# Optimization experiments

Hardware: AMD Instinct MI355X
Metric: run time of the kernel (lower is better)

The kernel has to match this reference:

```python
import jax, jax.numpy as jnp
import numpy as np

N_NODES = 50000
N_EDGES = 800000
NODE_DIM = 128
EDGE_DIM = 16
OUT_DIM = 64
HEADS = 4


def setup_inputs() -> dict:
    key = jax.random.key(0)
    ks = jax.random.split(key, 12)
    x = jax.random.normal(ks[0], (N_NODES, NODE_DIM), jnp.float32)
    edge_index = jax.random.randint(ks[1], (2, N_EDGES), 0, N_NODES)
    batch = jnp.zeros((N_NODES,), jnp.int32)
    edge_attr = jax.random.normal(ks[2], (N_EDGES, EDGE_DIM), jnp.float32)
    s = 1.0 / np.sqrt(NODE_DIM)
    W = jax.random.normal(ks[3], (NODE_DIM, HEADS * OUT_DIM), jnp.float32) * s
    att_src = jax.random.normal(ks[4], (HEADS, OUT_DIM), jnp.float32) * 0.1
    att_dst = jax.random.normal(ks[5], (HEADS, OUT_DIM), jnp.float32) * 0.1
    W_e = jax.random.normal(ks[6], (EDGE_DIM, HEADS * OUT_DIM), jnp.float32) * (1.0 / np.sqrt(EDGE_DIM))
    att_edge = jax.random.normal(ks[7], (HEADS, OUT_DIM), jnp.float32) * 0.1
    bias = jnp.zeros((OUT_DIM,), jnp.float32)
    gamma = jnp.ones((OUT_DIM,), jnp.float32)
    beta = jnp.zeros((OUT_DIM,), jnp.float32)
    return {"x": x, "edge_index": edge_index, "batch": batch, "edge_attr": edge_attr,
            "W": W, "att_src": att_src, "att_dst": att_dst, "W_e": W_e,
            "att_edge": att_edge, "bias": bias, "gamma": gamma, "beta": beta}


def reference(x, edge_index, batch, edge_attr, W, att_src, att_dst, W_e, att_edge, bias, gamma, beta):
    N = x.shape[0]
    H, C = att_src.shape
    src, dst = edge_index[0], edge_index[1]
    E = src.shape[0]

    # add self loops; self-loop edge_attr = per-node mean of incoming edge attrs (PyG fill_value='mean')
    cnt = jax.ops.segment_sum(jnp.ones((E, 1), x.dtype), dst, num_segments=N)
    loop_attr = jax.ops.segment_sum(edge_attr, dst, num_segments=N) / jnp.maximum(cnt, 1.0)
    loop_idx = jnp.arange(N, dtype=src.dtype)
    src_f = jnp.concatenate([src, loop_idx])
    dst_f = jnp.concatenate([dst, loop_idx])
    ea = jnp.concatenate([edge_attr, loop_attr], axis=0)

    h = (x @ W).reshape(N, H, C)                       # [N,H,C]
    a_src = jnp.einsum('nhc,hc->nh', h, att_src)       # [N,H]
    a_dst = jnp.einsum('nhc,hc->nh', h, att_dst)
    e_emb = (ea @ W_e).reshape(-1, H, C)               # [E',H,C]
    a_edge = jnp.einsum('ehc,hc->eh', e_emb, att_edge)

    alpha = jax.nn.leaky_relu(a_src[src_f] + a_dst[dst_f] + a_edge, 0.2)  # [E',H]
    amax = jax.ops.segment_max(alpha, dst_f, num_segments=N)
    expa = jnp.exp(alpha - amax[dst_f])
    denom = jax.ops.segment_sum(expa, dst_f, num_segments=N)
    att = expa / (denom[dst_f] + 1e-16)                # segment softmax over dst

    msg = h[src_f] * att[:, :, None]                   # [E',H,C]
    out = jax.ops.segment_sum(msg, dst_f, num_segments=N)  # [N,H,C]
    out = out.mean(axis=1) + bias                      # concat=False -> head mean

    mu = out.mean(-1, keepdims=True)
    var = out.var(-1, keepdims=True)
    out = (out - mu) / jnp.sqrt(var + 1e-5) * gamma + beta
    return jax.nn.elu(out)
```

## Files before the change

### kernel.cpp

```cpp
#include <hip/hip_runtime.h>

typedef unsigned int u32;
typedef unsigned short u16;

static constexpr int NN  = 50000;
static constexpr int EE  = 800000;
static constexpr int CAP = 64;

typedef __attribute__((ext_vector_type(8))) short bf16x8;
typedef __attribute__((ext_vector_type(4))) float f32x4;

__device__ inline float u2f(u32 u){ union{u32 i; float f;} v; v.i=u; return v.f; }
__device__ inline float bf2f(u16 u){ return u2f(((u32)u)<<16); }
__device__ inline u16 f2bf(float f){ union{float f; u32 i;} v; v.f=f; u32 i=v.i;
    return (u16)((i + 0x7fffu + ((i>>16)&1u))>>16); }
__device__ inline u32 pk2(float a, float b){ return (u32)f2bf(a) | ((u32)f2bf(b)<<16); }
__device__ inline float lrelu(float x){ return x > 0.f ? x : 0.2f*x; }

__device__ inline float ld(const void* base, size_t i, int f32m){
    return f32m ? ((const float*)base)[i] : bf2f(((const u16*)base)[i]);
}

__device__ inline float wsum(float v){
    #pragma unroll
    for (int m=1;m<64;m<<=1) v += __shfl_xor(v, m, 64);
    return v;
}

#if defined(__has_builtin)
#if __has_builtin(__builtin_amdgcn_fdot2_f32_bf16)
#define HAS_DOT2 1
#endif
#endif

#ifdef HAS_DOT2
typedef __attribute__((ext_vector_type(2))) __bf16 bf16x2;
#endif

__device__ inline float dot2acc(u32 hv, u32 wv, float acc){
#ifdef HAS_DOT2
    union { u32 u; bf16x2 v; } a, b; a.u = hv; b.u = wv;
    return __builtin_amdgcn_fdot2_f32_bf16(a.v, b.v, acc, false);
#else
    acc = fmaf(u2f(hv<<16),         u2f(wv<<16),         acc);
    acc = fmaf(u2f(hv&0xffff0000u), u2f(wv&0xffff0000u), acc);
    return acc;
#endif
}

__device__ inline int detect_f32(const u16* xraw){
    int lane = threadIdx.x & 63;
    bool bad = false;
    #pragma unroll
    for (int i = 0; i < 8; ++i){
        float v = bf2f(xraw[2*(lane + i*64)]);
        if (!(fabsf(v) < 1e10f)) bad = true;
    }
    return __any(bad) ? 1 : 0;
}

__device__ inline void edge_logits(const void* ea, int e, int f32m,
                                   const float* Ml, float* A){
    float v[16];
    if (f32m){
        const float4* r = ((const float4*)ea) + (size_t)e*4;
        float4 a = r[0], b = r[1], c = r[2], d = r[3];
        v[0]=a.x; v[1]=a.y; v[2]=a.z; v[3]=a.w;
        v[4]=b.x; v[5]=b.y; v[6]=b.z; v[7]=b.w;
        v[8]=c.x; v[9]=c.y; v[10]=c.z; v[11]=c.w;
        v[12]=d.x; v[13]=d.y; v[14]=d.z; v[15]=d.w;
    } else {
        const uint4* r = ((const uint4*)ea) + (size_t)e*2;
        uint4 q0 = r[0], q1 = r[1];
        v[0]=u2f(q0.x<<16); v[1]=u2f(q0.x&0xffff0000u);
        v[2]=u2f(q0.y<<16); v[3]=u2f(q0.y&0xffff0000u);
        v[4]=u2f(q0.z<<16); v[5]=u2f(q0.z&0xffff0000u);
        v[6]=u2f(q0.w<<16); v[7]=u2f(q0.w&0xffff0000u);
        v[8]=u2f(q1.x<<16); v[9]=u2f(q1.x&0xffff0000u);
        v[10]=u2f(q1.y<<16); v[11]=u2f(q1.y&0xffff0000u);
        v[12]=u2f(q1.z<<16); v[13]=u2f(q1.z&0xffff0000u);
        v[14]=u2f(q1.w<<16); v[15]=u2f(q1.w&0xffff0000u);
    }
    float a0=0,a1=0,a2=0,a3=0;
    #pragma unroll
    for (int j = 0; j < 16; ++j){
        a0 = fmaf(v[j], Ml[j*4+0], a0);
        a1 = fmaf(v[j], Ml[j*4+1], a1);
        a2 = fmaf(v[j], Ml[j*4+2], a2);
        a3 = fmaf(v[j], Ml[j*4+3], a3);
    }
    A[0]=a0; A[1]=a1; A[2]=a2; A[3]=a3;
}

__global__ __launch_bounds__(256) void k_prep(const u16* __restrict__ xraw,
                                              const void* __restrict__ W,
                                              const void* __restrict__ att_src,
                                              const void* __restrict__ att_dst,
                                              const void* __restrict__ W_e,
                                              const void* __restrict__ att_edge,
                                              int* __restrict__ flag,
                                              u16* __restrict__ Wt,
                                              float* __restrict__ Mv){
    int f32m = detect_f32(xraw);
    int b = blockIdx.x, t = threadIdx.x;
    if (b == 0){
        if (t == 0) *flag = f32m;
        if (t < 64){
            int d = t >> 2, h = t & 3;
            float s = 0.f;
            for (int c = 0; c < 64; ++c)
                s += ld(W_e, d*256 + h*64 + c, f32m) * ld(att_edge, h*64 + c, f32m);
            Mv[t] = s;
        }
    } else if (b <= 128){
        int i = (b-1)*256 + t;
        int k = i >> 8, n = i & 255;
        Wt[n*128 + k] = f2bf(ld(W, (size_t)k*256 + n, f32m));
    } else {
        int i = (b-129)*256 + t;
        int c = i >> 7, k = i & 127;
        float s = 0.f;
        if (c < 8){
            int h = c & 3;
            const void* att = (c < 4) ? att_src : att_dst;
            for (int j = 0; j < 64; ++j)
                s += ld(W, (size_t)k*256 + h*64 + j, f32m) * ld(att, h*64 + j, f32m);
        }
        Wt[(size_t)(256 + c)*128 + k] = f2bf(s);
    }
}

static constexpr int LDSROW = 136;
static constexpr int CROW   = 264;

__global__ __launch_bounds__(256) void k_gemm(const void* __restrict__ x,
                                              const u16* __restrict__ Wt,
                                              const int* __restrict__ flag,
                                              u16* __restrict__ hbuf,
                                              float* __restrict__ a_src,
                                              float* __restrict__ a_dst, int N){
    __shared__ u16 sh[64*CROW];
    int f32m = *flag;
    int t = threadIdx.x;
    int row0 = blockIdx.x*64;
    if (f32m){
        const float4* xg = (const float4*)x;
        #pragma unroll
        for (int j=0;j<8;++j){
            int idx = t + j*256;
            int r = idx >> 5, c4 = idx & 31;
            int gr = row0 + r; if (gr >= N) gr = N-1;
            float4 v = xg[(size_t)gr*32 + c4];
            *(uint2*)&sh[r*LDSROW + c4*4] = make_uint2(pk2(v.x,v.y), pk2(v.z,v.w));
        }
    } else {
        const uint4* xg = (const uint4*)x;
        #pragma unroll
        for (int j=0;j<4;++j){
            int idx = t + j*256;
            int r = idx >> 4, c8 = idx & 15;
            int gr = row0 + r; if (gr >= N) gr = N-1;
            uint4 v = xg[(size_t)gr*16 + c8];
            *(uint4*)&sh[r*LDSROW + c8*8] = v;
        }
    }
    __syncthreads();
    int wave = t >> 6, lane = t & 63;
    int l15 = lane & 15, quad = lane >> 4;
    int mrow = wave*16 + l15;
    bf16x8 afr[4];
    #pragma unroll
    for (int s=0;s<4;++s)
        afr[s] = *(const bf16x8*)&sh[mrow*LDSROW + s*32 + quad*8];
    __syncthreads();
    f32x4 acc[17];
    #pragma unroll
    for (int tl=0;tl<17;++tl){
        f32x4 a = {0.f,0.f,0.f,0.f};
        #pragma unroll
        for (int s=0;s<4;++s){
            bf16x8 bfr = *(const bf16x8*)&Wt[(size_t)(tl*16 + l15)*128 + s*32 + quad*8];
            a = __builtin_amdgcn_mfma_f32_16x16x32_bf16(afr[s], bfr, a, 0, 0, 0);
        }
        acc[tl] = a;
    }
    int rbase = row0 + wave*16 + quad*4;
    #pragma unroll
    for (int r=0;r<4;++r){
        int gr = rbase + r;
        if (gr < N){
            if (l15 < 4)      a_src[gr*4 + l15]     = acc[16][r];
            else if (l15 < 8) a_dst[gr*4 + (l15-4)] = acc[16][r];
        }
    }
    #pragma unroll
    for (int r=0;r<4;++r){
        int row = wave*16 + quad*4 + r;
        #pragma unroll
        for (int tl=0;tl<4;++tl){
            u32 lo = pk2(acc[tl  ][r], acc[tl+4 ][r]);
            u32 hi = pk2(acc[tl+8][r], acc[tl+12][r]);
            *(uint2*)&sh[row*CROW + (tl*16 + l15)*4] = make_uint2(lo, hi);
        }
    }
    __syncthreads();
    uint4* h4 = (uint4*)hbuf;
    #pragma unroll
    for (int j=0;j<8;++j){
        int idx = t + j*256;
        int row = idx >> 5, c16 = idx & 31;
        if (row0 + row < N){
            uint4 v = *(const uint4*)&sh[row*CROW + c16*8];
            h4[(size_t)(row0 + row)*32 + c16] = v;
        }
    }
}

__global__ __launch_bounds__(256) void k_edge(const int* __restrict__ ei,
                                              const void* __restrict__ ea,
                                              const float* __restrict__ Mv,
                                              const int* __restrict__ flag,
                                              const float* __restrict__ a_src,
                                              const float* __restrict__ a_dst,
                                              int* __restrict__ deg,
                                              uint4* __restrict__ brec,
                                              u32* __restrict__ ba23, int E){
    __shared__ float Ml[64];
    if (threadIdx.x < 64) Ml[threadIdx.x] = Mv[threadIdx.x];
    __syncthreads();
    int f32m = *flag;
    int base = blockIdx.x*1024 + threadIdx.x;
    int e[4], src[4], dst[4];
    bool val[4];
    float A[4][4];
    #pragma unroll
    for (int j=0;j<4;++j){
        e[j] = base + j*256;
        val[j] = e[j] < E;
        int ec = val[j] ? e[j] : 0;
        src[j] = ei[ec];
        dst[j] = ei[E + ec];
        edge_logits(ea, ec, f32m, Ml, A[j]);
    }
    float4 as[4], ad[4];
    #pragma unroll
    for (int j=0;j<4;++j){
        as[j] = ((const float4*)a_src)[src[j]];
        ad[j] = ((const float4*)a_dst)[dst[j]];
    }
    #pragma unroll
    for (int j=0;j<4;++j){
        if (!val[j]) continue;
        float w0 = expf(lrelu(as[j].x + ad[j].x + A[j][0]));
        float w1 = expf(lrelu(as[j].y + ad[j].y + A[j][1]));
        float w2 = expf(lrelu(as[j].z + ad[j].z + A[j][2]));
        float w3 = expf(lrelu(as[j].w + ad[j].w + A[j][3]));
        int slot = atomicAdd(&deg[dst[j]], 1);
        if (slot < CAP){
            int idx = dst[j]*CAP + slot;
            brec[idx] = make_uint4((u32)src[j], pk2(w0,w1), pk2(w2,w3), pk2(A[j][0],A[j][1]));
            ba23[idx] = pk2(A[j][2],A[j][3]);
        }
    }
}

__global__ __launch_bounds__(256) void k_node(const int* __restrict__ deg,
                                              const uint4* __restrict__ brec,
                                              const u32* __restrict__ ba23,
                                              const float* __restrict__ a_src,
                                              const float* __restrict__ a_dst,
                                              const u16* __restrict__ hbuf,
                                              const void* __restrict__ bias,
                                              const void* __restrict__ gamma,
                                              const void* __restrict__ beta,
                                              const int* __restrict__ flag,
                                              void* __restrict__ out, int N){
    __shared__ uint4 lrec[4][CAP+4];
    int f32m = *flag;
    int lane = threadIdx.x & 63;
    int slot = threadIdx.x >> 6;
    int n = blockIdx.x*4 + slot;
    int dg = deg[n];
    int dc = dg < CAP ? dg : CAP;
    float4 an = ((const float4*)a_src)[n];
    float4 ad = ((const float4*)a_dst)[n];
    bool v0 = lane < dc;
    u32 src = (u32)n;
    float w0=0.f,w1=0.f,w2=0.f,w3=0.f;
    float a0=0.f,a1=0.f,a2=0.f,a3=0.f;
    if (v0){
        uint4 r = brec[(size_t)n*CAP + lane];
        u32 q = ba23[(size_t)n*CAP + lane];
        src = r.x;
        w0 = u2f(r.y<<16); w1 = u2f(r.y&0xffff0000u);
        w2 = u2f(r.z<<16); w3 = u2f(r.z&0xffff0000u);
        a0 = u2f(r.w<<16); a1 = u2f(r.w&0xffff0000u);
        a2 = u2f(q<<16);   a3 = u2f(q&0xffff0000u);
    }
    float dn0 = wsum(w0), dn1 = wsum(w1), dn2 = wsum(w2), dn3 = wsum(w3);
    float invd = 1.f / (float)(dg > 1 ? dg : 1);
    float ge0 = wsum(a0)*invd, ge1 = wsum(a1)*invd;
    float ge2 = wsum(a2)*invd, ge3 = wsum(a3)*invd;
    float exS0 = expf(lrelu(an.x + ad.x + ge0));
    float exS1 = expf(lrelu(an.y + ad.y + ge1));
    float exS2 = expf(lrelu(an.z + ad.z + ge2));
    float exS3 = expf(lrelu(an.w + ad.w + ge3));
    float i0 = 0.25f/(dn0 + exS0 + 1e-16f);
    float i1 = 0.25f/(dn1 + exS1 + 1e-16f);
    float i2 = 0.25f/(dn2 + exS2 + 1e-16f);
    float i3 = 0.25f/(dn3 + exS3 + 1e-16f);
    if (v0)
        lrec[slot][lane] = make_uint4(src, pk2(w0*i0, w1*i1), pk2(w2*i2, w3*i3), 0u);
    if (lane == 0)
        lrec[slot][dc] = make_uint4((u32)n, pk2(exS0*i0, exS1*i1), pk2(exS2*i2, exS3*i3), 0u);
    else if (lane <= 3)
        lrec[slot][dc + lane] = make_uint4((u32)n, 0u, 0u, 0u);
    __syncthreads();
    int T = dc + 1;
    int iters = (T + 3) >> 2;
    int half = lane >> 5, l5 = lane & 31;
    const uint4* hb4 = (const uint4*)hbuf;
    float acc0 = 0.f, acc1 = 0.f;
    uint4 r0 = lrec[slot][half];
    uint4 r1 = lrec[slot][2 + half];
    uint4 h0 = hb4[(size_t)r0.x*32 + l5];
    uint4 h1 = hb4[(size_t)r1.x*32 + l5];
    for (int i = 1; i < iters; ++i){
        uint4 nr0 = lrec[slot][4*i + half];
        uint4 nr1 = lrec[slot][4*i + 2 + half];
        uint4 nh0 = hb4[(size_t)nr0.x*32 + l5];
        uint4 nh1 = hb4[(size_t)nr1.x*32 + l5];
        acc0 = dot2acc(h0.x, r0.y, acc0);
        acc0 = dot2acc(h0.y, r0.z, acc0);
        acc1 = dot2acc(h0.z, r0.y, acc1);
        acc1 = dot2acc(h0.w, r0.z, acc1);
        acc0 = dot2acc(h1.x, r1.y, acc0);
        acc0 = dot2acc(h1.y, r1.z, acc0);
        acc1 = dot2acc(h1.z, r1.y, acc1);
        acc1 = dot2acc(h1.w, r1.z, acc1);
        r0 = nr0; r1 = nr1; h0 = nh0; h1 = nh1;
    }
    acc0 = dot2acc(h0.x, r0.y, acc0);
    acc0 = dot2acc(h0.y, r0.z, acc0);
    acc1 = dot2acc(h0.z, r0.y, acc1);
    acc1 = dot2acc(h0.w, r0.z, acc1);
    acc0 = dot2acc(h1.x, r1.y, acc0);
    acc0 = dot2acc(h1.y, r1.z, acc0);
    acc1 = dot2acc(h1.z, r1.y, acc1);
    acc1 = dot2acc(h1.w, r1.z, acc1);
    acc0 += __shfl_xor(acc0, 32, 64);
    acc1 += __shfl_xor(acc1, 32, 64);
    float va = __shfl(acc0, lane>>1, 64);
    float vb = __shfl(acc1, lane>>1, 64);
    float o = ((lane & 1) ? vb : va) + ld(bias, lane, f32m);
    float mu = wsum(o) * (1.f/64.f);
    float d = o - mu;
    float var = wsum(d*d) * (1.f/64.f);
    float y = d * rsqrtf(var + 1e-5f) * ld(gamma, lane, f32m) + ld(beta, lane, f32m);
    y = y > 0.f ? y : expf(y) - 1.f;
    if (f32m) ((float*)out)[(size_t)n*64 + lane] = y;
    else      ((u16*)out)[(size_t)n*64 + lane] = f2bf(y);
}

extern "C" void kernel_launch(void* const* d_in, const int* in_sizes, int n_in,
                              void* d_out, int out_size, void* d_ws, size_t ws_size,
                              hipStream_t stream){
    const void* x        = d_in[0];
    const int*  ei       = (const int*)d_in[1];
    const void* ea       = d_in[3];
    const void* W        = d_in[4];
    const void* att_src  = d_in[5];
    const void* att_dst  = d_in[6];
    const void* W_e      = d_in[7];
    const void* att_edge = d_in[8];
    const void* bias     = d_in[9];
    const void* gamma    = d_in[10];
    const void* beta     = d_in[11];
    const int N = NN, E = EE;

    char* p = (char*)d_ws;
    auto alloc = [&](size_t bytes){ void* r = (void*)p; p += (bytes + 255) & ~(size_t)255; return r; };
    int*   deg   = (int*)  alloc((size_t)N*4);
    float* Mv    = (float*)alloc(64*4);
    float* a_src = (float*)alloc((size_t)N*16);
    float* a_dst = (float*)alloc((size_t)N*16);
    uint4* brec  = (uint4*)alloc((size_t)N*CAP*16);
    u32*   ba23  = (u32*)  alloc((size_t)N*CAP*4);
    u16*   hbuf  = (u16*)  alloc((size_t)N*256*2);
    u16*   Wt    = (u16*)  alloc((size_t)272*128*2);
    int*   flag  = (int*)  alloc(256);

    hipMemsetAsync(deg, 0, (size_t)N*4, stream);
    k_prep<<<137, 256, 0, stream>>>((const u16*)x, W, att_src, att_dst, W_e, att_edge,
                                    flag, Wt, Mv);
    k_gemm<<<(N+63)/64, 256, 0, stream>>>(x, Wt, flag, hbuf, a_src, a_dst, N);
    k_edge<<<(E+1023)/1024, 256, 0, stream>>>(ei, ea, Mv, flag, a_src, a_dst,
                                              deg, brec, ba23, E);
    k_node<<<N/4, 256, 0, stream>>>(deg, brec, ba23, a_src, a_dst, hbuf,
                                    bias, gamma, beta, flag, d_out, N);
}
```

Measured before the change: 299.7 us.

## Pre-convert edge attributes to bf16 in prep kernel and slim edge kernel

Adds blocks to the prep kernel that convert edge_attr into a packed bf16 buffer, or copy it when it is already bf16. The edge kernel then reads half-width rows without a dtype branch. It also processes 2 edges per thread instead of 4, sets a launch-bounds occupancy hint, and uses __expf in the edge and node kernels. The aim is to cut the edge kernel's attribute read bandwidth and register pressure. In exchange it adds a separate read-and-write pass over edge_attr plus bf16 rounding of the edge attributes.

```diff
diff --git a/kernel.cpp b/kernel.cpp
--- a/kernel.cpp
+++ b/kernel.cpp
@@ -59,48 +59,17 @@
     return __any(bad) ? 1 : 0;
 }
 
-__device__ inline void edge_logits(const void* ea, int e, int f32m,
-                                   const float* Ml, float* A){
-    float v[16];
-    if (f32m){
-        const float4* r = ((const float4*)ea) + (size_t)e*4;
-        float4 a = r[0], b = r[1], c = r[2], d = r[3];
-        v[0]=a.x; v[1]=a.y; v[2]=a.z; v[3]=a.w;
-        v[4]=b.x; v[5]=b.y; v[6]=b.z; v[7]=b.w;
-        v[8]=c.x; v[9]=c.y; v[10]=c.z; v[11]=c.w;
-        v[12]=d.x; v[13]=d.y; v[14]=d.z; v[15]=d.w;
-    } else {
-        const uint4* r = ((const uint4*)ea) + (size_t)e*2;
-        uint4 q0 = r[0], q1 = r[1];
-        v[0]=u2f(q0.x<<16); v[1]=u2f(q0.x&0xffff0000u);
-        v[2]=u2f(q0.y<<16); v[3]=u2f(q0.y&0xffff0000u);
-        v[4]=u2f(q0.z<<16); v[5]=u2f(q0.z&0xffff0000u);
-        v[6]=u2f(q0.w<<16); v[7]=u2f(q0.w&0xffff0000u);
-        v[8]=u2f(q1.x<<16); v[9]=u2f(q1.x&0xffff0000u);
-        v[10]=u2f(q1.y<<16); v[11]=u2f(q1.y&0xffff0000u);
-        v[12]=u2f(q1.z<<16); v[13]=u2f(q1.z&0xffff0000u);
-        v[14]=u2f(q1.w<<16); v[15]=u2f(q1.w&0xffff0000u);
-    }
-    float a0=0,a1=0,a2=0,a3=0;
-    #pragma unroll
-    for (int j = 0; j < 16; ++j){
-        a0 = fmaf(v[j], Ml[j*4+0], a0);
-        a1 = fmaf(v[j], Ml[j*4+1], a1);
-        a2 = fmaf(v[j], Ml[j*4+2], a2);
-        a3 = fmaf(v[j], Ml[j*4+3], a3);
-    }
-    A[0]=a0; A[1]=a1; A[2]=a2; A[3]=a3;
-}
-
 __global__ __launch_bounds__(256) void k_prep(const u16* __restrict__ xraw,
                                               const void* __restrict__ W,
                                               const void* __restrict__ att_src,
                                               const void* __restrict__ att_dst,
                                               const void* __restrict__ W_e,
                                               const void* __restrict__ att_edge,
+                                              const void* __restrict__ ea,
                                               int* __restrict__ flag,
                                               u16* __restrict__ Wt,
-                                              float* __restrict__ Mv){
+                                              float* __restrict__ Mv,
+                                              u16* __restrict__ eab){
     int f32m = detect_f32(xraw);
     int b = blockIdx.x, t = threadIdx.x;
     if (b == 0){
@@ -116,7 +85,7 @@
         int i = (b-1)*256 + t;
         int k = i >> 8, n = i & 255;
         Wt[n*128 + k] = f2bf(ld(W, (size_t)k*256 + n, f32m));
-    } else {
+    } else if (b <= 136){
         int i = (b-129)*256 + t;
         int c = i >> 7, k = i & 127;
         float s = 0.f;
@@ -127,6 +96,28 @@
                 s += ld(W, (size_t)k*256 + h*64 + j, f32m) * ld(att, h*64 + j, f32m);
         }
         Wt[(size_t)(256 + c)*128 + k] = f2bf(s);
+    } else {
+        int ci0 = (b-137)*2048 + t;
+        uint4* dst4 = (uint4*)eab;
+        if (f32m){
+            const uint4* s4 = (const uint4*)ea;
+            #pragma unroll
+            for (int j = 0; j < 8; ++j){
+                int ci = ci0 + j*256;
+                if (ci < EE*2){
+                    uint4 w0 = s4[2*ci], w1 = s4[2*ci+1];
+                    dst4[ci] = make_uint4(pk2(u2f(w0.x),u2f(w0.y)), pk2(u2f(w0.z),u2f(w0.w)),
+                                          pk2(u2f(w1.x),u2f(w1.y)), pk2(u2f(w1.z),u2f(w1.w)));
+                }
+            }
+        } else {
+            const uint4* s4 = (const uint4*)ea;
+            #pragma unroll
+            for (int j = 0; j < 8; ++j){
+                int ci = ci0 + j*256;
+                if (ci < EE*2) dst4[ci] = s4[ci];
+            }
+        }
     }
 }
 
@@ -216,45 +207,55 @@
     }
 }
 
-__global__ __launch_bounds__(256) void k_edge(const int* __restrict__ ei,
-                                              const void* __restrict__ ea,
-                                              const float* __restrict__ Mv,
-                                              const int* __restrict__ flag,
-                                              const float* __restrict__ a_src,
-                                              const float* __restrict__ a_dst,
-                                              int* __restrict__ deg,
-                                              uint4* __restrict__ brec,
-                                              u32* __restrict__ ba23, int E){
+__global__ __launch_bounds__(256, 6) void k_edge(const int* __restrict__ ei,
+                                                 const u16* __restrict__ eab,
+                                                 const float* __restrict__ Mv,
+                                                 const float* __restrict__ a_src,
+                                                 const float* __restrict__ a_dst,
+                                                 int* __restrict__ deg,
+                                                 uint4* __restrict__ brec,
+                                                 u32* __restrict__ ba23, int E){
     __shared__ float Ml[64];
     if (threadIdx.x < 64) Ml[threadIdx.x] = Mv[threadIdx.x];
     __syncthreads();
-    int f32m = *flag;
-    int base = blockIdx.x*1024 + threadIdx.x;
-    int e[4], src[4], dst[4];
-    bool val[4];
-    float A[4][4];
-    #pragma unroll
-    for (int j=0;j<4;++j){
-        e[j] = base + j*256;
-        val[j] = e[j] < E;
-        int ec = val[j] ? e[j] : 0;
+    int base = blockIdx.x*512 + threadIdx.x;
+    const uint4* e4 = (const uint4*)eab;
+    int src[2], dst[2];
+    bool val[2];
+    float A[2][4];
+    #pragma unroll
+    for (int j=0;j<2;++j){
+        int e = base + j*256;
+        val[j] = e < E;
+        int ec = val[j] ? e : 0;
         src[j] = ei[ec];
         dst[j] = ei[E + ec];
-        edge_logits(ea, ec, f32m, Ml, A[j]);
-    }
-    float4 as[4], ad[4];
-    #pragma unroll
-    for (int j=0;j<4;++j){
+        uint4 qa = e4[2*ec], qb = e4[2*ec+1];
+        u32 w[8] = {qa.x,qa.y,qa.z,qa.w,qb.x,qb.y,qb.z,qb.w};
+        float a0=0,a1=0,a2=0,a3=0;
+        #pragma unroll
+        for (int i=0;i<8;++i){
+            float v0 = u2f(w[i]<<16), v1 = u2f(w[i]&0xffff0000u);
+            a0 = fmaf(v0, Ml[(2*i)*4+0], fmaf(v1, Ml[(2*i+1)*4+0], a0));
+            a1 = fmaf(v0, Ml[(2*i)*4+1], fmaf(v1, Ml[(2*i+1)*4+1], a1));
+            a2 = fmaf(v0, Ml[(2*i)*4+2], fmaf(v1, Ml[(2*i+1)*4+2], a2));
+            a3 = fmaf(v0, Ml[(2*i)*4+3], fmaf(v1, Ml[(2*i+1)*4+3], a3));
+        }
+        A[j][0]=a0; A[j][1]=a1; A[j][2]=a2; A[j][3]=a3;
+    }
+    float4 as[2], ad[2];
+    #pragma unroll
+    for (int j=0;j<2;++j){
         as[j] = ((const float4*)a_src)[src[j]];
         ad[j] = ((const float4*)a_dst)[dst[j]];
     }
     #pragma unroll
-    for (int j=0;j<4;++j){
+    for (int j=0;j<2;++j){
         if (!val[j]) continue;
-        float w0 = expf(lrelu(as[j].x + ad[j].x + A[j][0]));
-        float w1 = expf(lrelu(as[j].y + ad[j].y + A[j][1]));
-        float w2 = expf(lrelu(as[j].z + ad[j].z + A[j][2]));
-        float w3 = expf(lrelu(as[j].w + ad[j].w + A[j][3]));
+        float w0 = __expf(lrelu(as[j].x + ad[j].x + A[j][0]));
+        float w1 = __expf(lrelu(as[j].y + ad[j].y + A[j][1]));
+        float w2 = __expf(lrelu(as[j].z + ad[j].z + A[j][2]));
+        float w3 = __expf(lrelu(as[j].w + ad[j].w + A[j][3]));
         int slot = atomicAdd(&deg[dst[j]], 1);
         if (slot < CAP){
             int idx = dst[j]*CAP + slot;
@@ -301,10 +302,10 @@
     float invd = 1.f / (float)(dg > 1 ? dg : 1);
     float ge0 = wsum(a0)*invd, ge1 = wsum(a1)*invd;
     float ge2 = wsum(a2)*invd, ge3 = wsum(a3)*invd;
-    float exS0 = expf(lrelu(an.x + ad.x + ge0));
-    float exS1 = expf(lrelu(an.y + ad.y + ge1));
-    float exS2 = expf(lrelu(an.z + ad.z + ge2));
-    float exS3 = expf(lrelu(an.w + ad.w + ge3));
+    float exS0 = __expf(lrelu(an.x + ad.x + ge0));
+    float exS1 = __expf(lrelu(an.y + ad.y + ge1));
+    float exS2 = __expf(lrelu(an.z + ad.z + ge2));
+    float exS3 = __expf(lrelu(an.w + ad.w + ge3));
     float i0 = 0.25f/(dn0 + exS0 + 1e-16f);
     float i1 = 0.25f/(dn1 + exS1 + 1e-16f);
     float i2 = 0.25f/(dn2 + exS2 + 1e-16f);
@@ -357,7 +358,7 @@
     float d = o - mu;
     float var = wsum(d*d) * (1.f/64.f);
     float y = d * rsqrtf(var + 1e-5f) * ld(gamma, lane, f32m) + ld(beta, lane, f32m);
-    y = y > 0.f ? y : expf(y) - 1.f;
+    y = y > 0.f ? y : __expf(y) - 1.f;
     if (f32m) ((float*)out)[(size_t)n*64 + lane] = y;
     else      ((u16*)out)[(size_t)n*64 + lane] = f2bf(y);
 }
@@ -388,14 +389,16 @@
     u32*   ba23  = (u32*)  alloc((size_t)N*CAP*4);
     u16*   hbuf  = (u16*)  alloc((size_t)N*256*2);
     u16*   Wt    = (u16*)  alloc((size_t)272*128*2);
+    u16*   eab   = (u16*)  alloc((size_t)E*16*2);
     int*   flag  = (int*)  alloc(256);
 
     hipMemsetAsync(deg, 0, (size_t)N*4, stream);
-    k_prep<<<137, 256, 0, stream>>>((const u16*)x, W, att_src, att_dst, W_e, att_edge,
-                                    flag, Wt, Mv);
+    int convBlocks = (E*2 + 2047) / 2048;
+    k_prep<<<137 + convBlocks, 256, 0, stream>>>((const u16*)x, W, att_src, att_dst,
+                                                 W_e, att_edge, ea, flag, Wt, Mv, eab);
     k_gemm<<<(N+63)/64, 256, 0, stream>>>(x, Wt, flag, hbuf, a_src, a_dst, N);
-    k_edge<<<(E+1023)/1024, 256, 0, stream>>>(ei, ea, Mv, flag, a_src, a_dst,
-                                              deg, brec, ba23, E);
+    k_edge<<<(E+511)/512, 256, 0, stream>>>(ei, eab, Mv, a_src, a_dst,
+                                            deg, brec, ba23, E);
     k_node<<<N/4, 256, 0, stream>>>(deg, brec, ba23, a_src, a_dst, hbuf,
                                     bias, gamma, beta, flag, d_out, N);
 }
```

Result: slower. 363.4 us (+21.2%).
